# Kernel optimization log

Hardware: AMD Instinct MI355X
Metric: run time of the kernel (lower is better)

The kernel has to match this reference:

```python
import jax, jax.numpy as jnp
import numpy as np

B, L, V, N = 2, 2048, 32000, 1024  # batch, seq, vocab, n_embd (ambient dim = N+1)


def _sanitize(x):
    return jnp.nan_to_num(x, nan=0.0, posinf=1e4, neginf=-1e4)


def _safe_acosh(x):
    # safe_acosh_v2: Taylor expansion near x=1 to avoid gradient explosion.
    xm1 = jnp.maximum(x - 1.0, 0.0)
    near = xm1 < 1e-3
    taylor = jnp.sqrt(2.0 * jnp.maximum(xm1, 1e-12)) * (1.0 - xm1 / 12.0)
    exact = jnp.arccosh(jnp.maximum(x, 1.0 + 1e-7))
    return jnp.where(near, taylor, exact)


def setup_inputs() -> dict:
    key = jax.random.key(0)
    k1, k2 = jax.random.split(key)
    # Build valid Lorentz points on H^n: x0 = sqrt(1 + ||x_spatial||^2)
    sp = 0.5 * jax.random.normal(k1, (B, L, N), dtype=jnp.float32)
    t = jnp.sqrt(1.0 + jnp.sum(sp * sp, axis=-1, keepdims=True))
    hidden_states = jnp.concatenate([t, sp], axis=-1)  # [B, L, N+1]
    weight = 0.01 * jax.random.normal(k2, (V, N), dtype=jnp.float32)  # tangent vectors
    logit_scale = jnp.asarray(1.0 / np.sqrt(N), dtype=jnp.float32)  # init_logit_scale/sqrt(n_embd)
    return {"hidden_states": hidden_states, "weight": weight, "logit_scale": logit_scale}


def reference(hidden_states, weight, logit_scale):
    h = _sanitize(hidden_states)
    # exp_map_zero of zero-padded tangent vectors [V, N] -> hyperboloid points [V, N+1]
    # exp_o(v) = cosh(||v||) * o + sinh(||v||)/||v|| * v, with o = (1, 0, ..., 0)
    norm = jnp.linalg.norm(weight, axis=-1)  # [V]
    r = jnp.where(norm > 1e-7, jnp.sinh(norm) / jnp.maximum(norm, 1e-7), 1.0)
    w_time = jnp.cosh(norm)          # [V]
    w_space = r[:, None] * weight    # [V, N]
    # Lorentz distance: d = acosh(-<h, w>_L), -<h,w>_L = h0*w0 - h_sp . w_sp
    # Expressed as a GEMM over the vocab instead of a [B,L,V,N+1] broadcast.
    x = h[..., :1] * w_time[None, None, :] - jnp.einsum('bln,vn->blv', h[..., 1:], w_space)
    d = _safe_acosh(x)  # [B, L, V]
    tau = jnp.clip(logit_scale, 0.01, 2.5)
    logits = -tau * d * d
    return _sanitize(logits)
```

## Files before the change

kernel.cpp:

```cpp
#include <hip/hip_runtime.h>
#include <hip/hip_bf16.h>
#include <hip/hip_fp8.h>
#include <math.h>

#define M_TOT 4096
#define K_TOT 1024
#define V_TOT 32000

typedef int int4v __attribute__((ext_vector_type(4)));
typedef int int8v __attribute__((ext_vector_type(8)));
typedef float f32x4 __attribute__((ext_vector_type(4)));

__device__ __forceinline__ void gload_lds16(const void* g, void* l) {
  __builtin_amdgcn_global_load_lds(
      (const __attribute__((address_space(1))) void*)g,
      (__attribute__((address_space(3))) void*)l, 16, 0, 0);
}

__device__ __forceinline__ float sani(float v) {
  return (v != v) ? 0.0f : fminf(fmaxf(v, -1e4f), 1e4f);
}

__device__ __forceinline__ int pk4_fp8(float a, float b, float c, float d) {
#if __has_builtin(__builtin_amdgcn_cvt_pk_fp8_f32)
  int p = __builtin_amdgcn_cvt_pk_fp8_f32(a, b, 0, false);
  p = __builtin_amdgcn_cvt_pk_fp8_f32(c, d, p, true);
  return p;
#else
  union { unsigned char b4[4]; int i; } u;
  u.b4[0] = __hip_fp8_e4m3(a).__x;
  u.b4[1] = __hip_fp8_e4m3(b).__x;
  u.b4[2] = __hip_fp8_e4m3(c).__x;
  u.b4[3] = __hip_fp8_e4m3(d).__x;
  return u.i;
#endif
}

__global__ void prep_hw(const float* __restrict__ h, const float* __restrict__ w,
                        unsigned char* __restrict__ h8, unsigned char* __restrict__ w8,
                        float* __restrict__ h0, float* __restrict__ wtime) {
  __shared__ float red[4];
  __shared__ float r_sh;
  const int b = blockIdx.x;
  const int t = threadIdx.x;
  if (b < M_TOT) {
    const int m = b;
    const float* row = h + (long)m * (K_TOT + 1);
    if (t == 0) h0[m] = sani(row[0]);
    float4 x = *(const float4*)(row + 1 + t * 4);
    ((int*)(h8 + (long)m * K_TOT))[t] =
        pk4_fp8(sani(x.x), sani(x.y), sani(x.z), sani(x.w));
  } else {
    const int v = b - M_TOT;
    const float* row = w + (long)v * K_TOT;
    float4 x = *(const float4*)(row + t * 4);
    float s = x.x * x.x + x.y * x.y + x.z * x.z + x.w * x.w;
#pragma unroll
    for (int off = 32; off > 0; off >>= 1) s += __shfl_down(s, off);
    int lane = t & 63, wv = t >> 6;
    if (lane == 0) red[wv] = s;
    __syncthreads();
    if (t == 0) {
      float tot = red[0] + red[1] + red[2] + red[3];
      float norm = sqrtf(tot);
      float r = (norm > 1e-7f) ? (sinhf(norm) / fmaxf(norm, 1e-7f)) : 1.0f;
      r_sh = r;
      wtime[v] = coshf(norm);
    }
    __syncthreads();
    float sc = 16.0f * r_sh;
    ((int*)(w8 + (long)v * K_TOT))[t] =
        pk4_fp8(sc * x.x, sc * x.y, sc * x.z, sc * x.w);
  }
}

#define BAR __builtin_amdgcn_s_barrier()
#define LGKM0 asm volatile("s_waitcnt lgkmcnt(0)" ::: "memory")
#define VM8 asm volatile("s_waitcnt vmcnt(8)" ::: "memory")

__global__ __launch_bounds__(512, 2) void gemm_geo(
    const unsigned char* __restrict__ h8, const unsigned char* __restrict__ w8,
    const float* __restrict__ h0, const float* __restrict__ wtime,
    const float* __restrict__ ls, float* __restrict__ out) {
  __shared__ __align__(16) char smem[131072];

  const int t = threadIdx.x;
  const int wave = t >> 6, lane = t & 63;
  const int fr = lane & 15, fq = lane >> 4;
  const int wm = wave >> 2, wn = wave & 3;

  const int bid = blockIdx.x;
  const int swz = (bid & 7) * 250 + (bid >> 3);
  const int tile_v = swz >> 4;
  const int mhalf = (swz >> 3) & 1;
  const int tile_m = (swz & 7) + mhalf * 8;
  const int row0 = tile_m * 256;
  const int col0 = tile_v * 256;

  const int xorv = fr & 7;
  const int c0 = ((2 * fq) ^ xorv) * 16;
  const int c1 = ((2 * fq + 1) ^ xorv) * 16;
  const int a_rd = (wm * 128 + fr) * 128;
  const int b_rd = 32768 + (wn * 64 + fr) * 128;

  auto RDF = [&](int off) -> int8v {
    int4v lo = *(const int4v*)(smem + off + c0);
    int4v hi = *(const int4v*)(smem + off + c1);
    return (int8v){lo[0], lo[1], lo[2], lo[3], hi[0], hi[1], hi[2], hi[3]};
  };

  const int cc = (t & 7) ^ ((t >> 3) & 7);
  const unsigned char* pA = h8 + ((long)row0 + (t >> 3)) * K_TOT + cc * 16;
  const unsigned char* pB = w8 + ((long)col0 + (t >> 3)) * K_TOT + cc * 16;
  const int dst_w = wave * 1024;

  auto STAGE = [&](int kt, int bufo) {
#pragma unroll
    for (int hh = 0; hh < 4; ++hh) {
      gload_lds16(pA + (long)hh * 65536 + kt * 128,
                  smem + bufo + hh * 8192 + dst_w);
      gload_lds16(pB + (long)hh * 65536 + kt * 128,
                  smem + bufo + 32768 + hh * 8192 + dst_w);
    }
  };

  f32x4 acc[8][4];
#pragma unroll
  for (int i = 0; i < 8; ++i)
#pragma unroll
    for (int j = 0; j < 4; ++j) acc[i][j] = (f32x4)(0.0f);

  STAGE(0, 0);
  STAGE(1, 65536);
  VM8;
  BAR;

#pragma unroll 1
  for (int kt = 0; kt < 8; ++kt) {
    const int cbo = (kt & 1) << 16;
    const int skt = (kt + 2 < 8) ? kt + 2 : 7;

    int8v bv[4], av[4];
#pragma unroll
    for (int iv = 0; iv < 4; ++iv) bv[iv] = RDF(cbo + b_rd + iv * 2048);
#pragma unroll
    for (int im = 0; im < 4; ++im) av[im] = RDF(cbo + a_rd + im * 2048);

    __builtin_amdgcn_s_setprio(1);
#pragma unroll
    for (int im = 0; im < 4; ++im)
#pragma unroll
      for (int iv = 0; iv < 4; ++iv)
        acc[im][iv] = __builtin_amdgcn_mfma_scale_f32_16x16x128_f8f6f4(
            bv[iv], av[im], acc[im][iv], 0, 0, 0, 0x7B7B7B7B, 0, 0x7F7F7F7F);
    __builtin_amdgcn_s_setprio(0);

    int8v av2[4];
#pragma unroll
    for (int im = 0; im < 4; ++im)
      av2[im] = RDF(cbo + a_rd + (4 + im) * 2048);
    LGKM0;
    __builtin_amdgcn_sched_barrier(0);
    BAR;

    STAGE(skt, cbo);

    __builtin_amdgcn_s_setprio(1);
#pragma unroll
    for (int im = 0; im < 4; ++im)
#pragma unroll
      for (int iv = 0; iv < 4; ++iv)
        acc[4 + im][iv] = __builtin_amdgcn_mfma_scale_f32_16x16x128_f8f6f4(
            bv[iv], av2[im], acc[4 + im][iv], 0, 0, 0, 0x7B7B7B7B, 0,
            0x7F7F7F7F);
    __builtin_amdgcn_s_setprio(0);

    VM8;
    BAR;
  }

  const float ntau = -fminf(fmaxf(ls[0], 0.01f), 2.5f);
  const float LN2 = 0.69314718055994531f;
  f32x4 wt4[4];
#pragma unroll
  for (int iv = 0; iv < 4; ++iv)
    wt4[iv] = *(const f32x4*)&wtime[col0 + wn * 64 + iv * 16 + fq * 4];
#pragma unroll
  for (int im = 0; im < 8; ++im) {
    const float hh = h0[row0 + wm * 128 + im * 16 + fr];
    float* orow =
        out + (long)(row0 + wm * 128 + im * 16 + fr) * V_TOT + col0 + wn * 64;
#pragma unroll
    for (int iv = 0; iv < 4; ++iv) {
      f32x4 r;
#pragma unroll
      for (int j = 0; j < 4; ++j) {
        float x = fmaf(hh, wt4[iv][j], -acc[im][iv][j]);
        float xm1 = fmaxf(x - 1.0f, 0.0f);
        float arg = fmaxf(fmaf(x, x, -1.0f), 0.0f);
        float lg2 = __builtin_amdgcn_logf(x + __builtin_amdgcn_sqrtf(arg));
        float dex = LN2 * lg2;
        float d2_exact = dex * dex;
        float ts = fmaf(xm1, -1.0f / 12.0f, 1.0f);
        float d2_tay = 2.0f * xm1 * ts * ts;
        float d2 = (xm1 < 1e-3f) ? d2_tay : d2_exact;
        r[j] = ntau * d2;
      }
      __builtin_nontemporal_store(r, (f32x4*)(orow + iv * 16 + fq * 4));
    }
  }
}

extern "C" void kernel_launch(void* const* d_in, const int* in_sizes, int n_in,
                              void* d_out, int out_size, void* d_ws, size_t ws_size,
                              hipStream_t stream) {
  const float* h = (const float*)d_in[0];
  const float* w = (const float*)d_in[1];
  const float* ls = (const float*)d_in[2];
  float* out = (float*)d_out;

  char* ws = (char*)d_ws;
  unsigned char* w8 = (unsigned char*)ws;
  unsigned char* h8 = (unsigned char*)(ws + 32768000);
  float* wtime = (float*)(ws + 32768000 + 4194304);
  float* h0 = (float*)(ws + 32768000 + 4194304 + 128000);

  prep_hw<<<M_TOT + V_TOT, 256, 0, stream>>>(h, w, h8, w8, h0, wtime);
  gemm_geo<<<2000, 512, 0, stream>>>(h8, w8, h0, wtime, ls, out);
}
```

Baseline: 277.0 us.

## Load B fragments directly from global into registers, shrink tile to 128x256

Restructures the FP8 GEMM so that only the A (hidden) tile is staged through LDS, double-buffered in 32KB. Each wave now loads its B (weight) MFMA fragments straight from global memory into registers. Tiles shrink to 128x256 with 256-thread blocks and 4000 blocks, and the block swizzle is reworked. The aim is to cut LDS traffic and footprint and raise occupancy, at the cost of redundant global/L2 reads of B across the M tiles and more vector registers.

```diff
diff --git a/kernel.cpp b/kernel.cpp
--- a/kernel.cpp
+++ b/kernel.cpp
@@ -75,124 +75,113 @@
 }
 
 #define BAR __builtin_amdgcn_s_barrier()
-#define LGKM0 asm volatile("s_waitcnt lgkmcnt(0)" ::: "memory")
-#define VM8 asm volatile("s_waitcnt vmcnt(8)" ::: "memory")
-
-__global__ __launch_bounds__(512, 2) void gemm_geo(
+#define VM16 asm volatile("s_waitcnt vmcnt(16)" ::: "memory")
+#define VM4 asm volatile("s_waitcnt vmcnt(4)" ::: "memory")
+
+__global__ __launch_bounds__(256, 2) void gemm_geo(
     const unsigned char* __restrict__ h8, const unsigned char* __restrict__ w8,
     const float* __restrict__ h0, const float* __restrict__ wtime,
     const float* __restrict__ ls, float* __restrict__ out) {
-  __shared__ __align__(16) char smem[131072];
+  __shared__ __align__(16) char smem[32768];
 
   const int t = threadIdx.x;
   const int wave = t >> 6, lane = t & 63;
   const int fr = lane & 15, fq = lane >> 4;
-  const int wm = wave >> 2, wn = wave & 3;
+  const int wm = wave >> 1, wn = wave & 1;
 
   const int bid = blockIdx.x;
-  const int swz = (bid & 7) * 250 + (bid >> 3);
-  const int tile_v = swz >> 4;
-  const int mhalf = (swz >> 3) & 1;
-  const int tile_m = (swz & 7) + mhalf * 8;
-  const int row0 = tile_m * 256;
+  const int swz = (bid & 7) * 500 + (bid >> 3);
+  const int g = swz >> 4;
+  const int sub = swz & 15;
+  const int half = (g >= 125) ? 1 : 0;
+  const int tile_v = g - half * 125;
+  const int tile_m = half * 16 + sub;
+  const int row0 = tile_m * 128;
   const int col0 = tile_v * 256;
 
   const int xorv = fr & 7;
   const int c0 = ((2 * fq) ^ xorv) * 16;
   const int c1 = ((2 * fq + 1) ^ xorv) * 16;
-  const int a_rd = (wm * 128 + fr) * 128;
-  const int b_rd = 32768 + (wn * 64 + fr) * 128;
-
-  auto RDF = [&](int off) -> int8v {
-    int4v lo = *(const int4v*)(smem + off + c0);
-    int4v hi = *(const int4v*)(smem + off + c1);
-    return (int8v){lo[0], lo[1], lo[2], lo[3], hi[0], hi[1], hi[2], hi[3]};
-  };
+  const int a_rd = (wm * 64 + fr) * 128;
 
   const int cc = (t & 7) ^ ((t >> 3) & 7);
   const unsigned char* pA = h8 + ((long)row0 + (t >> 3)) * K_TOT + cc * 16;
-  const unsigned char* pB = w8 + ((long)col0 + (t >> 3)) * K_TOT + cc * 16;
   const int dst_w = wave * 1024;
 
   auto STAGE = [&](int kt, int bufo) {
 #pragma unroll
-    for (int hh = 0; hh < 4; ++hh) {
-      gload_lds16(pA + (long)hh * 65536 + kt * 128,
-                  smem + bufo + hh * 8192 + dst_w);
-      gload_lds16(pB + (long)hh * 65536 + kt * 128,
-                  smem + bufo + 32768 + hh * 8192 + dst_w);
-    }
+    for (int hh = 0; hh < 4; ++hh)
+      gload_lds16(pA + (long)hh * (32L * K_TOT) + kt * 128,
+                  smem + bufo + hh * 4096 + dst_w);
   };
 
-  f32x4 acc[8][4];
-#pragma unroll
-  for (int i = 0; i < 8; ++i)
-#pragma unroll
-    for (int j = 0; j < 4; ++j) acc[i][j] = (f32x4)(0.0f);
+  const unsigned char* pB =
+      w8 + ((long)col0 + wn * 128 + fr) * K_TOT + fq * 32;
+
+  f32x4 acc[4][8];
+#pragma unroll
+  for (int i = 0; i < 4; ++i)
+#pragma unroll
+    for (int j = 0; j < 8; ++j) acc[i][j] = (f32x4)(0.0f);
 
   STAGE(0, 0);
-  STAGE(1, 65536);
-  VM8;
-  BAR;
 
 #pragma unroll 1
   for (int kt = 0; kt < 8; ++kt) {
-    const int cbo = (kt & 1) << 16;
-    const int skt = (kt + 2 < 8) ? kt + 2 : 7;
-
-    int8v bv[4], av[4];
-#pragma unroll
-    for (int iv = 0; iv < 4; ++iv) bv[iv] = RDF(cbo + b_rd + iv * 2048);
-#pragma unroll
-    for (int im = 0; im < 4; ++im) av[im] = RDF(cbo + a_rd + im * 2048);
+    const int cbo = (kt & 1) << 14;
+    const int nbo = cbo ^ 16384;
+    const int skt = (kt + 1 < 8) ? kt + 1 : 7;
+
+    int4v blo[8], bhi[8];
+#pragma unroll
+    for (int iv = 0; iv < 8; ++iv) {
+      const unsigned char* pb = pB + (long)iv * (16L * K_TOT) + kt * 128;
+      blo[iv] = *(const int4v*)pb;
+      bhi[iv] = *(const int4v*)(pb + 16);
+    }
+
+    VM16;
+    BAR;
+
+    STAGE(skt, nbo);
+
+    int8v av[4];
+#pragma unroll
+    for (int im = 0; im < 4; ++im) {
+      int4v lo = *(const int4v*)(smem + cbo + a_rd + im * 2048 + c0);
+      int4v hi = *(const int4v*)(smem + cbo + a_rd + im * 2048 + c1);
+      av[im] = (int8v){lo[0], lo[1], lo[2], lo[3], hi[0], hi[1], hi[2], hi[3]};
+    }
+
+    VM4;
 
     __builtin_amdgcn_s_setprio(1);
 #pragma unroll
     for (int im = 0; im < 4; ++im)
 #pragma unroll
-      for (int iv = 0; iv < 4; ++iv)
+      for (int iv = 0; iv < 8; ++iv) {
+        int8v bv = (int8v){blo[iv][0], blo[iv][1], blo[iv][2], blo[iv][3],
+                           bhi[iv][0], bhi[iv][1], bhi[iv][2], bhi[iv][3]};
         acc[im][iv] = __builtin_amdgcn_mfma_scale_f32_16x16x128_f8f6f4(
-            bv[iv], av[im], acc[im][iv], 0, 0, 0, 0x7B7B7B7B, 0, 0x7F7F7F7F);
+            bv, av[im], acc[im][iv], 0, 0, 0, 0x7B7B7B7B, 0, 0x7F7F7F7F);
+      }
     __builtin_amdgcn_s_setprio(0);
-
-    int8v av2[4];
-#pragma unroll
-    for (int im = 0; im < 4; ++im)
-      av2[im] = RDF(cbo + a_rd + (4 + im) * 2048);
-    LGKM0;
-    __builtin_amdgcn_sched_barrier(0);
-    BAR;
-
-    STAGE(skt, cbo);
-
-    __builtin_amdgcn_s_setprio(1);
-#pragma unroll
-    for (int im = 0; im < 4; ++im)
-#pragma unroll
-      for (int iv = 0; iv < 4; ++iv)
-        acc[4 + im][iv] = __builtin_amdgcn_mfma_scale_f32_16x16x128_f8f6f4(
-            bv[iv], av2[im], acc[4 + im][iv], 0, 0, 0, 0x7B7B7B7B, 0,
-            0x7F7F7F7F);
-    __builtin_amdgcn_s_setprio(0);
-
-    VM8;
-    BAR;
   }
 
   const float ntau = -fminf(fmaxf(ls[0], 0.01f), 2.5f);
   const float LN2 = 0.69314718055994531f;
-  f32x4 wt4[4];
-#pragma unroll
-  for (int iv = 0; iv < 4; ++iv)
-    wt4[iv] = *(const f32x4*)&wtime[col0 + wn * 64 + iv * 16 + fq * 4];
-#pragma unroll
-  for (int im = 0; im < 8; ++im) {
-    const float hh = h0[row0 + wm * 128 + im * 16 + fr];
-    float* orow =
-        out + (long)(row0 + wm * 128 + im * 16 + fr) * V_TOT + col0 + wn * 64;
-#pragma unroll
-    for (int iv = 0; iv < 4; ++iv) {
-      f32x4 r;
+  f32x4 wt4[8];
+#pragma unroll
+  for (int iv = 0; iv < 8; ++iv)
+    wt4[iv] = *(const f32x4*)&wtime[col0 + wn * 128 + iv * 16 + fq * 4];
+#pragma unroll
+  for (int im = 0; im < 4; ++im) {
+    const float hh = h0[row0 + wm * 64 + im * 16 + fr];
+    float* orow = out + (long)(row0 + wm * 64 + im * 16 + fr) * V_TOT + col0 +
+                  wn * 128;
+    f32x4 rv[8];
+#pragma unroll
+    for (int iv = 0; iv < 8; ++iv) {
 #pragma unroll
       for (int j = 0; j < 4; ++j) {
         float x = fmaf(hh, wt4[iv][j], -acc[im][iv][j]);
@@ -204,10 +193,12 @@
         float ts = fmaf(xm1, -1.0f / 12.0f, 1.0f);
         float d2_tay = 2.0f * xm1 * ts * ts;
         float d2 = (xm1 < 1e-3f) ? d2_tay : d2_exact;
-        r[j] = ntau * d2;
+        rv[iv][j] = ntau * d2;
       }
-      __builtin_nontemporal_store(r, (f32x4*)(orow + iv * 16 + fq * 4));
-    }
+    }
+#pragma unroll
+    for (int iv = 0; iv < 8; ++iv)
+      __builtin_nontemporal_store(rv[iv], (f32x4*)(orow + iv * 16 + fq * 4));
   }
 }
 
@@ -226,5 +217,5 @@
   float* h0 = (float*)(ws + 32768000 + 4194304 + 128000);
 
   prep_hw<<<M_TOT + V_TOT, 256, 0, stream>>>(h, w, h8, w8, h0, wtime);
-  gemm_geo<<<2000, 512, 0, stream>>>(h8, w8, h0, wtime, ls, out);
-}
+  gemm_geo<<<4000, 256, 0, stream>>>(h8, w8, h0, wtime, ls, out);
+}
```

Result: slower. 358.6 us (+29.5%).
